# Performance work log

Measured on AMD Instinct MI355X. Metric: run time of the kernel, lower is better.

Reference implementation:

```python
import jax, jax.numpy as jnp
import numpy as np

N_HEAD = 12

def setup_inputs() -> dict:
    key = jax.random.key(0)
    k1, k2, k3, k4, k5 = jax.random.split(key, 5)
    B, T, C = 2, 2048, 768
    x = jax.random.normal(k1, (B, T, C), dtype=jnp.float32)
    W_attn = jax.random.normal(k2, (C, 3 * C), dtype=jnp.float32) * 0.02
    b_attn = jax.random.normal(k3, (3 * C,), dtype=jnp.float32) * 0.02
    W_proj = jax.random.normal(k4, (C, C), dtype=jnp.float32) * 0.02
    b_proj = jax.random.normal(k5, (C,), dtype=jnp.float32) * 0.02
    return {"x": x, "W_attn": W_attn, "b_attn": b_attn, "W_proj": W_proj, "b_proj": b_proj}

def reference(x, W_attn, b_attn, W_proj, b_proj):
    B, T, C = x.shape
    H = N_HEAD
    hd = C // H
    qkv = x @ W_attn + b_attn  # [B,T,3C]
    q, k, v = jnp.split(qkv, 3, axis=2)
    # [B,H,T,hd]
    q = q.reshape(B, T, H, hd).transpose(0, 2, 1, 3)
    k = k.reshape(B, T, H, hd).transpose(0, 2, 1, 3)
    v = v.reshape(B, T, H, hd).transpose(0, 2, 1, 3)
    att = jnp.einsum('bhqd,bhkd->bhqk', q, k) / jnp.sqrt(jnp.float32(hd))
    causal = jnp.tril(jnp.ones((T, T), dtype=bool))
    att = jnp.where(causal[None, None], att, -jnp.inf)
    att = jax.nn.softmax(att, axis=-1)
    y = jnp.einsum('bhqk,bhkd->bhqd', att, v)  # [B,H,T,hd]
    y = y.transpose(0, 2, 1, 3).reshape(B, T, C)
    return y @ W_proj + b_proj
```

## Files before the change

kernel.cpp:

```cpp
#include <hip/hip_runtime.h>
#include <stdint.h>

typedef unsigned short u16;
typedef __attribute__((ext_vector_type(8))) short bf16x8;
typedef __attribute__((ext_vector_type(4))) float f32x4;

__device__ __forceinline__ u16 f2bf(float f){
  union { float f; uint32_t u; } v; v.f = f;
  uint32_t u = v.u;
  u += 0x7FFFu + ((u >> 16) & 1u);
  return (u16)(u >> 16);
}

__device__ __forceinline__ float fexp2(float x){
#if __has_builtin(__builtin_amdgcn_exp2f)
  return __builtin_amdgcn_exp2f(x);
#else
  return exp2f(x);
#endif
}

__device__ __forceinline__ uint32_t cvtpk_bf16(float lo, float hi){
  uint32_t d;
  asm("v_cvt_pk_bf16_f32 %0, %1, %2" : "=v"(d) : "v"(lo), "v"(hi));
  return d;
}

__device__ __forceinline__ f32x4 mfma_bf16(bf16x8 a, bf16x8 b, f32x4 c){
  return __builtin_amdgcn_mfma_f32_16x16x32_bf16(a, b, c, 0, 0, 0);
}

#define QSCALE 0.1803368801111244f

__global__ __launch_bounds__(256) void cast_x_k(const float* __restrict__ x,
                                                u16* __restrict__ xb, int n4){
  int i = blockIdx.x*256 + threadIdx.x;
  if (i >= n4) return;
  float4 v = reinterpret_cast<const float4*>(x)[i];
  uint2 o;
  o.x = (uint32_t)f2bf(v.x) | ((uint32_t)f2bf(v.y) << 16);
  o.y = (uint32_t)f2bf(v.z) | ((uint32_t)f2bf(v.w) << 16);
  reinterpret_cast<uint2*>(xb)[i] = o;
}

__global__ __launch_bounds__(256) void transpose_cast_k(const float* __restrict__ in,
                                                        u16* __restrict__ out,
                                                        int R, int C){
  __shared__ u16 tile[64][66];
  int c0 = blockIdx.x*64, r0 = blockIdx.y*64;
  int tc = threadIdx.x & 63, t4 = threadIdx.x >> 6;
  #pragma unroll
  for (int i=0;i<16;i++){ int r = t4 + i*4; tile[r][tc] = f2bf(in[(size_t)(r0+r)*C + c0 + tc]); }
  __syncthreads();
  #pragma unroll
  for (int i=0;i<16;i++){ int cc = t4 + i*4; out[(size_t)(c0+cc)*R + r0 + tc] = tile[tc][cc]; }
}

#define LDP 40

template<int MFRAG>
__global__ __launch_bounds__(256) void gemm_bf16_k(
    const u16* __restrict__ A, const u16* __restrict__ Bt,
    int M, int N, int K, const float* __restrict__ bias, int mode,
    u16* __restrict__ qo, u16* __restrict__ ko, u16* __restrict__ vo,
    float* __restrict__ fo)
{
  constexpr int BM = MFRAG*32;
  __shared__ u16 As[BM*LDP];
  __shared__ u16 Bs[128*LDP];
  const int m0 = blockIdx.y*BM, n0 = blockIdx.x*128;
  const int tid = threadIdx.x, lane = tid & 63, wid = tid >> 6;
  const int lr = lane & 15, lg = lane >> 4;
  const int wr = wid >> 1, wc = wid & 1;
  f32x4 acc[MFRAG][4] = {};
  const int nk = K >> 5;
  for (int kk = 0; kk < nk; ++kk){
    #pragma unroll
    for (int s = 0; s < MFRAG/2; ++s){
      int ci = tid + 256*s;
      int row = ci >> 2, ch = ci & 3;
      *(uint4*)&As[row*LDP + ch*8] = *(const uint4*)&A[(size_t)(m0+row)*K + kk*32 + ch*8];
    }
    #pragma unroll
    for (int s = 0; s < 2; ++s){
      int ci = tid + 256*s;
      int row = ci >> 2, ch = ci & 3;
      *(uint4*)&Bs[row*LDP + ch*8] = *(const uint4*)&Bt[(size_t)(n0+row)*K + kk*32 + ch*8];
    }
    __syncthreads();
    bf16x8 af[MFRAG], bfr[4];
    #pragma unroll
    for (int m=0;m<MFRAG;m++) af[m] = *(const bf16x8*)&As[(wr*(MFRAG*16) + m*16 + lr)*LDP + lg*8];
    #pragma unroll
    for (int n=0;n<4;n++) bfr[n] = *(const bf16x8*)&Bs[(wc*64 + n*16 + lr)*LDP + lg*8];
    #pragma unroll
    for (int m=0;m<MFRAG;m++)
      #pragma unroll
      for (int n=0;n<4;n++)
        acc[m][n] = mfma_bf16(af[m], bfr[n], acc[m][n]);
    __syncthreads();
  }
  if (mode == 0){
    #pragma unroll
    for (int m=0;m<MFRAG;m++)
      #pragma unroll
      for (int n=0;n<4;n++){
        int gn = n0 + wc*64 + n*16 + lr;
        float bv = bias[gn];
        #pragma unroll
        for (int r=0;r<4;r++){
          int gm = m0 + wr*(MFRAG*16) + m*16 + lg*4 + r;
          fo[(size_t)gm*N + gn] = acc[m][n][r] + bv;
        }
      }
  } else {
    int which = n0 / 768;
    u16* dst = (which==0) ? qo : ko;
    float sc = (which==0) ? QSCALE : 1.0f;
    #pragma unroll
    for (int m=0;m<MFRAG;m++)
      #pragma unroll
      for (int n=0;n<4;n++){
        int gn = n0 + wc*64 + n*16 + lr;
        float bv = bias[gn];
        int cn = gn - which*768;
        int h = cn >> 6, d = cn & 63;
        int gm0 = m0 + wr*(MFRAG*16) + m*16 + lg*4;
        int b = gm0 >> 11, t0 = gm0 & 2047;
        if (which < 2){
          #pragma unroll
          for (int r=0;r<4;r++)
            dst[(size_t)((b*12 + h)*2048 + t0 + r)*64 + d] = f2bf((acc[m][n][r] + bv)*sc);
        } else {
          uint2 o;
          o.x = cvtpk_bf16(acc[m][n][0]+bv, acc[m][n][1]+bv);
          o.y = cvtpk_bf16(acc[m][n][2]+bv, acc[m][n][3]+bv);
          *(uint2*)&vo[((size_t)((b*12 + h)*64 + d))*2048 + t0] = o;
        }
      }
  }
}

__global__ __launch_bounds__(256) void attn_k(
    const u16* __restrict__ qp, const u16* __restrict__ kp,
    const u16* __restrict__ vtp, u16* __restrict__ yp)
{
  __shared__ f32x4 ylh[16][64];
  __shared__ float llh[4][16];
  const int i = blockIdx.x;
  const int bh = i % 24;
  const int qb = 63 - (i / 24);
  const int q0 = qb * 32;
  const int q0A = q0, q0B = q0 + 16;
  const int b = bh / 12, h = bh - b*12;
  const size_t base = (size_t)bh * 131072;
  const int tid = threadIdx.x, lane = tid & 63, wid = tid >> 6;
  const int lr = lane & 15, lg = lane >> 4;
  const int qgA = q0A + lr, qgB = q0B + lr;
  const u16* kbase = kp + base;
  const u16* vbase = vtp + base;

  bf16x8 qfA[2], qfB[2];
  #pragma unroll
  for (int kb=0;kb<2;kb++){
    qfA[kb] = *(const bf16x8*)&qp[base + (size_t)qgA*64 + kb*32 + lg*8];
    qfB[kb] = *(const bf16x8*)&qp[base + (size_t)qgB*64 + kb*32 + lg*8];
  }

  f32x4 yA[4] = {}, yB[4] = {};
  float lA = 0.f, lB = 0.f;
  const float m2 = 8.f;
  const int nt = (qb >> 1) + 1;

  uint32_t ko[8], vo[8];
  #pragma unroll
  for (int nb=0;nb<4;nb++){
    int ke = ((nb&1)*32 + (lr>>2)*8 + (nb>>1)*4 + (lr&3))*64 + lg*8;
    ko[nb*2+0] = (uint32_t)(wid*4096 + ke) * 2u;
    ko[nb*2+1] = (uint32_t)(wid*4096 + ke + 32) * 2u;
  }
  #pragma unroll
  for (int n=0;n<4;n++){
    int ve = (n*16+lr)*2048 + lg*8 + wid*64;
    vo[n*2+0] = (uint32_t)ve * 2u;
    vo[n*2+1] = (uint32_t)(ve + 32) * 2u;
  }

  for (int t = wid; t < nt; t += 4){
    bf16x8 kf[8], vf[8];
    #pragma unroll
    for (int j=0;j<8;j++) kf[j] = *(const bf16x8*)((const char*)kbase + ko[j]);
    #pragma unroll
    for (int j=0;j<8;j++) vf[j] = *(const bf16x8*)((const char*)vbase + vo[j]);
    #pragma unroll
    for (int j=0;j<8;j++){ ko[j] += 32768u; vo[j] += 512u; }

    const int k0 = t*64;
    const int nbmin[4] = {0, 32, 4, 36};

    uint32_t pkA[8], pkB[8];
    auto half_qk = [&](int q0H, int qgH, const bf16x8 (&qfH)[2],
                       float &lH, uint32_t (&pkH)[8]){
      f32x4 s[4] = {};
      __builtin_amdgcn_s_setprio(1);
      if (k0      <= q0H + 15){ s[0]=mfma_bf16(kf[0],qfH[0],s[0]); s[0]=mfma_bf16(kf[1],qfH[1],s[0]); }
      if (k0 + 32 <= q0H + 15){ s[1]=mfma_bf16(kf[2],qfH[0],s[1]); s[1]=mfma_bf16(kf[3],qfH[1],s[1]); }
      if (k0 +  4 <= q0H + 15){ s[2]=mfma_bf16(kf[4],qfH[0],s[2]); s[2]=mfma_bf16(kf[5],qfH[1],s[2]); }
      if (k0 + 36 <= q0H + 15){ s[3]=mfma_bf16(kf[6],qfH[0],s[3]); s[3]=mfma_bf16(kf[7],qfH[1],s[3]); }
      __builtin_amdgcn_s_setprio(0);
      if (k0 + 63 > q0H){
        #pragma unroll
        for (int nb=0;nb<4;nb++){
          int kb0 = k0 + (nb&1)*32 + ((nb>>1)&1)*4 + lg*8;
          #pragma unroll
          for (int r=0;r<4;r++)
            if (kb0 + r > qgH) s[nb][r] = -1e30f;
        }
      }
      float lsum = 0.f;
      #pragma unroll
      for (int nb=0;nb<4;nb++){
        if (k0 + nbmin[nb] <= q0H + 15){
          #pragma unroll
          for (int r=0;r<4;r++){
            float p = fexp2(s[nb][r] - m2);
            s[nb][r] = p;
            lsum += p;
          }
        } else {
          #pragma unroll
          for (int r=0;r<4;r++) s[nb][r] = 0.f;
        }
      }
      lH += lsum;
      #pragma unroll
      for (int nb=0;nb<4;nb++){
        pkH[nb*2]   = cvtpk_bf16(s[nb][0], s[nb][1]);
        pkH[nb*2+1] = cvtpk_bf16(s[nb][2], s[nb][3]);
      }
    };
    half_qk(q0A, qgA, qfA, lA, pkA);
    half_qk(q0B, qgB, qfB, lB, pkB);

    __builtin_amdgcn_s_setprio(1);
    {
      union { uint32_t u[4]; bf16x8 v; } pb;
      pb.u[0]=pkA[0]; pb.u[1]=pkA[1]; pb.u[2]=pkA[4]; pb.u[3]=pkA[5];
      yA[0]=mfma_bf16(vf[0],pb.v,yA[0]); yA[1]=mfma_bf16(vf[2],pb.v,yA[1]);
      yA[2]=mfma_bf16(vf[4],pb.v,yA[2]); yA[3]=mfma_bf16(vf[6],pb.v,yA[3]);
      pb.u[0]=pkA[2]; pb.u[1]=pkA[3]; pb.u[2]=pkA[6]; pb.u[3]=pkA[7];
      yA[0]=mfma_bf16(vf[1],pb.v,yA[0]); yA[1]=mfma_bf16(vf[3],pb.v,yA[1]);
      yA[2]=mfma_bf16(vf[5],pb.v,yA[2]); yA[3]=mfma_bf16(vf[7],pb.v,yA[3]);
      pb.u[0]=pkB[0]; pb.u[1]=pkB[1]; pb.u[2]=pkB[4]; pb.u[3]=pkB[5];
      yB[0]=mfma_bf16(vf[0],pb.v,yB[0]); yB[1]=mfma_bf16(vf[2],pb.v,yB[1]);
      yB[2]=mfma_bf16(vf[4],pb.v,yB[2]); yB[3]=mfma_bf16(vf[6],pb.v,yB[3]);
      pb.u[0]=pkB[2]; pb.u[1]=pkB[3]; pb.u[2]=pkB[6]; pb.u[3]=pkB[7];
      yB[0]=mfma_bf16(vf[1],pb.v,yB[0]); yB[1]=mfma_bf16(vf[3],pb.v,yB[1]);
      yB[2]=mfma_bf16(vf[5],pb.v,yB[2]); yB[3]=mfma_bf16(vf[7],pb.v,yB[3]);
    }
    __builtin_amdgcn_s_setprio(0);
  }

  lA += __shfl_xor(lA, 16);  lA += __shfl_xor(lA, 32);
  lB += __shfl_xor(lB, 16);  lB += __shfl_xor(lB, 32);

  #pragma unroll
  for (int hf=0; hf<2; hf++){
    if (hf) __syncthreads();
    #pragma unroll
    for (int n=0;n<4;n++) ylh[wid*4+n][lane] = hf ? yB[n] : yA[n];
    if (lg == 0) llh[wid][lr] = hf ? lB : lA;
    __syncthreads();
    float Ls = (llh[0][lr] + llh[1][lr]) + (llh[2][lr] + llh[3][lr]);
    f32x4 y0 = ylh[0*4+wid][lane], y1 = ylh[1*4+wid][lane],
          y2 = ylh[2*4+wid][lane], y3 = ylh[3*4+wid][lane];
    f32x4 ys;
    #pragma unroll
    for (int r=0;r<4;r++) ys[r] = (y0[r] + y1[r]) + (y2[r] + y3[r]);
    float inv = 1.0f / Ls;
    uint2 o;
    o.x = cvtpk_bf16(ys[0]*inv, ys[1]*inv);
    o.y = cvtpk_bf16(ys[2]*inv, ys[3]*inv);
    *(uint2*)&yp[(size_t)(b*2048 + q0 + hf*16 + lr)*768 + h*64 + wid*16 + lg*4] = o;
  }
}

extern "C" void kernel_launch(void* const* d_in, const int* in_sizes, int n_in,
                              void* d_out, int out_size, void* d_ws, size_t ws_size,
                              hipStream_t stream)
{
  const float* x  = (const float*)d_in[0];
  const float* Wa = (const float*)d_in[1];
  const float* ba = (const float*)d_in[2];
  const float* Wp = (const float*)d_in[3];
  const float* bp = (const float*)d_in[4];
  float* out = (float*)d_out;
  char* ws = (char*)d_ws;
  u16* xb  = (u16*)(ws + 0);
  u16* wt  = (u16*)(ws + 6291456);
  u16* wpt = (u16*)(ws + 9830400);
  u16* qb  = (u16*)(ws + 11010048);
  u16* kb  = (u16*)(ws + 17301504);
  u16* vtb = (u16*)(ws + 23592960);
  u16* yb  = (u16*)(ws + 29884416);

  cast_x_k<<<3072, 256, 0, stream>>>(x, xb, 786432);
  transpose_cast_k<<<dim3(36,12), 256, 0, stream>>>(Wa, wt, 768, 2304);
  transpose_cast_k<<<dim3(12,12), 256, 0, stream>>>(Wp, wpt, 768, 768);
  gemm_bf16_k<2><<<dim3(18,64), 256, 0, stream>>>(xb, wt, 4096, 2304, 768, ba, 1,
                                                  qb, kb, vtb, nullptr);
  attn_k<<<1536, 256, 0, stream>>>(qb, kb, vtb, yb);
  gemm_bf16_k<2><<<dim3(6,64), 256, 0, stream>>>(yb, wpt, 4096, 768, 768, bp, 0,
                                                 nullptr, nullptr, nullptr, out);
}
```

Baseline: 129.0 us.

## Persistent attention with atomic work queue; merge prep casts into one kernel

The three cast and transpose kernels are merged into a single prep kernel, which also zeroes eight work counters. The attention kernel becomes persistent with 1024 blocks. Each block pulls (query-block, head) tasks from one of eight atomic counters, heaviest query blocks first, so work balances dynamically across CUs instead of relying on a static grid. This adds an atomic and a barrier per task, and makes the attention kernel depend on the counters being reset by the prep kernel.

```diff
diff --git a/kernel.cpp b/kernel.cpp
--- a/kernel.cpp
+++ b/kernel.cpp
@@ -32,23 +32,31 @@
 
 #define QSCALE 0.1803368801111244f
 
-__global__ __launch_bounds__(256) void cast_x_k(const float* __restrict__ x,
-                                                u16* __restrict__ xb, int n4){
-  int i = blockIdx.x*256 + threadIdx.x;
-  if (i >= n4) return;
-  float4 v = reinterpret_cast<const float4*>(x)[i];
-  uint2 o;
-  o.x = (uint32_t)f2bf(v.x) | ((uint32_t)f2bf(v.y) << 16);
-  o.y = (uint32_t)f2bf(v.z) | ((uint32_t)f2bf(v.w) << 16);
-  reinterpret_cast<uint2*>(xb)[i] = o;
-}
-
-__global__ __launch_bounds__(256) void transpose_cast_k(const float* __restrict__ in,
-                                                        u16* __restrict__ out,
-                                                        int R, int C){
+__global__ __launch_bounds__(256) void prep_k(
+    const float* __restrict__ x,  u16* __restrict__ xb,
+    const float* __restrict__ Wa, u16* __restrict__ wt,
+    const float* __restrict__ Wp, u16* __restrict__ wpt,
+    uint32_t* __restrict__ cnt)
+{
   __shared__ u16 tile[64][66];
-  int c0 = blockIdx.x*64, r0 = blockIdx.y*64;
-  int tc = threadIdx.x & 63, t4 = threadIdx.x >> 6;
+  const int bid = blockIdx.x;
+  if (bid < 3072){
+    if (bid == 0 && threadIdx.x < 8) cnt[threadIdx.x] = 0u;
+    int i = bid*256 + threadIdx.x;
+    float4 v = reinterpret_cast<const float4*>(x)[i];
+    uint2 o;
+    o.x = (uint32_t)f2bf(v.x) | ((uint32_t)f2bf(v.y) << 16);
+    o.y = (uint32_t)f2bf(v.z) | ((uint32_t)f2bf(v.w) << 16);
+    reinterpret_cast<uint2*>(xb)[i] = o;
+    return;
+  }
+  const float* in; u16* out; int C, j;
+  if (bid < 3504){ j = bid - 3072; in = Wa; out = wt;  C = 2304; }
+  else           { j = bid - 3504; in = Wp; out = wpt; C = 768;  }
+  const int R = 768;
+  const int nbx = C >> 6;
+  const int c0 = (j % nbx) * 64, r0 = (j / nbx) * 64;
+  const int tc = threadIdx.x & 63, t4 = threadIdx.x >> 6;
   #pragma unroll
   for (int i=0;i<16;i++){ int r = t4 + i*4; tile[r][tc] = f2bf(in[(size_t)(r0+r)*C + c0 + tc]); }
   __syncthreads();
@@ -143,145 +151,160 @@
 
 __global__ __launch_bounds__(256) void attn_k(
     const u16* __restrict__ qp, const u16* __restrict__ kp,
-    const u16* __restrict__ vtp, u16* __restrict__ yp)
+    const u16* __restrict__ vtp, u16* __restrict__ yp,
+    uint32_t* __restrict__ cnt)
 {
   __shared__ f32x4 ylh[16][64];
   __shared__ float llh[4][16];
-  const int i = blockIdx.x;
-  const int bh = i % 24;
-  const int qb = 63 - (i / 24);
-  const int q0 = qb * 32;
-  const int q0A = q0, q0B = q0 + 16;
-  const int b = bh / 12, h = bh - b*12;
-  const size_t base = (size_t)bh * 131072;
+  __shared__ uint32_t task_s;
+  const int qid = blockIdx.x & 7;
   const int tid = threadIdx.x, lane = tid & 63, wid = tid >> 6;
   const int lr = lane & 15, lg = lane >> 4;
-  const int qgA = q0A + lr, qgB = q0B + lr;
-  const u16* kbase = kp + base;
-  const u16* vbase = vtp + base;
-
-  bf16x8 qfA[2], qfB[2];
+
+  int ke[4], ve[4];
   #pragma unroll
-  for (int kb=0;kb<2;kb++){
-    qfA[kb] = *(const bf16x8*)&qp[base + (size_t)qgA*64 + kb*32 + lg*8];
-    qfB[kb] = *(const bf16x8*)&qp[base + (size_t)qgB*64 + kb*32 + lg*8];
-  }
-
-  f32x4 yA[4] = {}, yB[4] = {};
-  float lA = 0.f, lB = 0.f;
-  const float m2 = 8.f;
-  const int nt = (qb >> 1) + 1;
-
-  uint32_t ko[8], vo[8];
+  for (int nb=0;nb<4;nb++)
+    ke[nb] = ((nb&1)*32 + (lr>>2)*8 + ((nb>>1)&1)*4 + (lr&3))*64 + lg*8;
   #pragma unroll
-  for (int nb=0;nb<4;nb++){
-    int ke = ((nb&1)*32 + (lr>>2)*8 + (nb>>1)*4 + (lr&3))*64 + lg*8;
-    ko[nb*2+0] = (uint32_t)(wid*4096 + ke) * 2u;
-    ko[nb*2+1] = (uint32_t)(wid*4096 + ke + 32) * 2u;
-  }
-  #pragma unroll
-  for (int n=0;n<4;n++){
-    int ve = (n*16+lr)*2048 + lg*8 + wid*64;
-    vo[n*2+0] = (uint32_t)ve * 2u;
-    vo[n*2+1] = (uint32_t)(ve + 32) * 2u;
-  }
-
-  for (int t = wid; t < nt; t += 4){
-    bf16x8 kf[8], vf[8];
-    #pragma unroll
-    for (int j=0;j<8;j++) kf[j] = *(const bf16x8*)((const char*)kbase + ko[j]);
-    #pragma unroll
-    for (int j=0;j<8;j++) vf[j] = *(const bf16x8*)((const char*)vbase + vo[j]);
-    #pragma unroll
-    for (int j=0;j<8;j++){ ko[j] += 32768u; vo[j] += 512u; }
-
-    const int k0 = t*64;
-    const int nbmin[4] = {0, 32, 4, 36};
-
-    uint32_t pkA[8], pkB[8];
-    auto half_qk = [&](int q0H, int qgH, const bf16x8 (&qfH)[2],
-                       float &lH, uint32_t (&pkH)[8]){
-      f32x4 s[4] = {};
-      __builtin_amdgcn_s_setprio(1);
-      if (k0      <= q0H + 15){ s[0]=mfma_bf16(kf[0],qfH[0],s[0]); s[0]=mfma_bf16(kf[1],qfH[1],s[0]); }
-      if (k0 + 32 <= q0H + 15){ s[1]=mfma_bf16(kf[2],qfH[0],s[1]); s[1]=mfma_bf16(kf[3],qfH[1],s[1]); }
-      if (k0 +  4 <= q0H + 15){ s[2]=mfma_bf16(kf[4],qfH[0],s[2]); s[2]=mfma_bf16(kf[5],qfH[1],s[2]); }
-      if (k0 + 36 <= q0H + 15){ s[3]=mfma_bf16(kf[6],qfH[0],s[3]); s[3]=mfma_bf16(kf[7],qfH[1],s[3]); }
-      __builtin_amdgcn_s_setprio(0);
-      if (k0 + 63 > q0H){
+  for (int n=0;n<4;n++)
+    ve[n] = (n*16+lr)*2048 + lg*8;
+
+  for (;;){
+    if (tid == 0) task_s = atomicAdd(&cnt[qid], 1u);
+    __syncthreads();
+    const uint32_t m = task_s;
+    if (m >= 192u) return;
+    const int qb = 63 - (int)(m / 3u);
+    const int bh = qid + 8 * (int)(m % 3u);
+    const int q0 = qb * 32;
+    const int q0A = q0, q0B = q0 + 16;
+    const int b = bh / 12, h = bh - b*12;
+    const size_t base = (size_t)bh * 131072;
+    const int qgA = q0A + lr, qgB = q0B + lr;
+    const u16* kbase = kp + base;
+    const u16* vbase = vtp + base;
+
+    bf16x8 qfA[2], qfB[2];
+    #pragma unroll
+    for (int kb=0;kb<2;kb++){
+      qfA[kb] = *(const bf16x8*)&qp[base + (size_t)qgA*64 + kb*32 + lg*8];
+      qfB[kb] = *(const bf16x8*)&qp[base + (size_t)qgB*64 + kb*32 + lg*8];
+    }
+
+    f32x4 yA[4] = {}, yB[4] = {};
+    float lA = 0.f, lB = 0.f;
+    const float m2 = 8.f;
+    const int nt = (qb >> 1) + 1;
+
+    uint32_t ko[8], vo[8];
+    #pragma unroll
+    for (int nb=0;nb<4;nb++){
+      ko[nb*2+0] = (uint32_t)(wid*4096 + ke[nb]) * 2u;
+      ko[nb*2+1] = (uint32_t)(wid*4096 + ke[nb] + 32) * 2u;
+    }
+    #pragma unroll
+    for (int n=0;n<4;n++){
+      vo[n*2+0] = (uint32_t)(ve[n] + wid*64) * 2u;
+      vo[n*2+1] = (uint32_t)(ve[n] + wid*64 + 32) * 2u;
+    }
+
+    for (int t = wid; t < nt; t += 4){
+      bf16x8 kf[8], vf[8];
+      #pragma unroll
+      for (int j=0;j<8;j++) kf[j] = *(const bf16x8*)((const char*)kbase + ko[j]);
+      #pragma unroll
+      for (int j=0;j<8;j++) vf[j] = *(const bf16x8*)((const char*)vbase + vo[j]);
+      #pragma unroll
+      for (int j=0;j<8;j++){ ko[j] += 32768u; vo[j] += 512u; }
+
+      const int k0 = t*64;
+      const int nbmin[4] = {0, 32, 4, 36};
+
+      uint32_t pkA[8], pkB[8];
+      auto half_qk = [&](int q0H, int qgH, const bf16x8 (&qfH)[2],
+                         float &lH, uint32_t (&pkH)[8]){
+        f32x4 s[4] = {};
+        __builtin_amdgcn_s_setprio(1);
+        if (k0      <= q0H + 15){ s[0]=mfma_bf16(kf[0],qfH[0],s[0]); s[0]=mfma_bf16(kf[1],qfH[1],s[0]); }
+        if (k0 + 32 <= q0H + 15){ s[1]=mfma_bf16(kf[2],qfH[0],s[1]); s[1]=mfma_bf16(kf[3],qfH[1],s[1]); }
+        if (k0 +  4 <= q0H + 15){ s[2]=mfma_bf16(kf[4],qfH[0],s[2]); s[2]=mfma_bf16(kf[5],qfH[1],s[2]); }
+        if (k0 + 36 <= q0H + 15){ s[3]=mfma_bf16(kf[6],qfH[0],s[3]); s[3]=mfma_bf16(kf[7],qfH[1],s[3]); }
+        __builtin_amdgcn_s_setprio(0);
+        if (k0 + 63 > q0H){
+          #pragma unroll
+          for (int nb=0;nb<4;nb++){
+            int kb0 = k0 + (nb&1)*32 + ((nb>>1)&1)*4 + lg*8;
+            #pragma unroll
+            for (int r=0;r<4;r++)
+              if (kb0 + r > qgH) s[nb][r] = -1e30f;
+          }
+        }
+        float lsum = 0.f;
         #pragma unroll
         for (int nb=0;nb<4;nb++){
-          int kb0 = k0 + (nb&1)*32 + ((nb>>1)&1)*4 + lg*8;
-          #pragma unroll
-          for (int r=0;r<4;r++)
-            if (kb0 + r > qgH) s[nb][r] = -1e30f;
-        }
+          if (k0 + nbmin[nb] <= q0H + 15){
+            #pragma unroll
+            for (int r=0;r<4;r++){
+              float p = fexp2(s[nb][r] - m2);
+              s[nb][r] = p;
+              lsum += p;
+            }
+          } else {
+            #pragma unroll
+            for (int r=0;r<4;r++) s[nb][r] = 0.f;
+          }
+        }
+        lH += lsum;
+        #pragma unroll
+        for (int nb=0;nb<4;nb++){
+          pkH[nb*2]   = cvtpk_bf16(s[nb][0], s[nb][1]);
+          pkH[nb*2+1] = cvtpk_bf16(s[nb][2], s[nb][3]);
+        }
+      };
+      half_qk(q0A, qgA, qfA, lA, pkA);
+      half_qk(q0B, qgB, qfB, lB, pkB);
+
+      __builtin_amdgcn_s_setprio(1);
+      {
+        union { uint32_t u[4]; bf16x8 v; } pb;
+        pb.u[0]=pkA[0]; pb.u[1]=pkA[1]; pb.u[2]=pkA[4]; pb.u[3]=pkA[5];
+        yA[0]=mfma_bf16(vf[0],pb.v,yA[0]); yA[1]=mfma_bf16(vf[2],pb.v,yA[1]);
+        yA[2]=mfma_bf16(vf[4],pb.v,yA[2]); yA[3]=mfma_bf16(vf[6],pb.v,yA[3]);
+        pb.u[0]=pkA[2]; pb.u[1]=pkA[3]; pb.u[2]=pkA[6]; pb.u[3]=pkA[7];
+        yA[0]=mfma_bf16(vf[1],pb.v,yA[0]); yA[1]=mfma_bf16(vf[3],pb.v,yA[1]);
+        yA[2]=mfma_bf16(vf[5],pb.v,yA[2]); yA[3]=mfma_bf16(vf[7],pb.v,yA[3]);
+        pb.u[0]=pkB[0]; pb.u[1]=pkB[1]; pb.u[2]=pkB[4]; pb.u[3]=pkB[5];
+        yB[0]=mfma_bf16(vf[0],pb.v,yB[0]); yB[1]=mfma_bf16(vf[2],pb.v,yB[1]);
+        yB[2]=mfma_bf16(vf[4],pb.v,yB[2]); yB[3]=mfma_bf16(vf[6],pb.v,yB[3]);
+        pb.u[0]=pkB[2]; pb.u[1]=pkB[3]; pb.u[2]=pkB[6]; pb.u[3]=pkB[7];
+        yB[0]=mfma_bf16(vf[1],pb.v,yB[0]); yB[1]=mfma_bf16(vf[3],pb.v,yB[1]);
+        yB[2]=mfma_bf16(vf[5],pb.v,yB[2]); yB[3]=mfma_bf16(vf[7],pb.v,yB[3]);
       }
-      float lsum = 0.f;
-      #pragma unroll
-      for (int nb=0;nb<4;nb++){
-        if (k0 + nbmin[nb] <= q0H + 15){
-          #pragma unroll
-          for (int r=0;r<4;r++){
-            float p = fexp2(s[nb][r] - m2);
-            s[nb][r] = p;
-            lsum += p;
-          }
-        } else {
-          #pragma unroll
-          for (int r=0;r<4;r++) s[nb][r] = 0.f;
-        }
-      }
-      lH += lsum;
-      #pragma unroll
-      for (int nb=0;nb<4;nb++){
-        pkH[nb*2]   = cvtpk_bf16(s[nb][0], s[nb][1]);
-        pkH[nb*2+1] = cvtpk_bf16(s[nb][2], s[nb][3]);
-      }
-    };
-    half_qk(q0A, qgA, qfA, lA, pkA);
-    half_qk(q0B, qgB, qfB, lB, pkB);
-
-    __builtin_amdgcn_s_setprio(1);
-    {
-      union { uint32_t u[4]; bf16x8 v; } pb;
-      pb.u[0]=pkA[0]; pb.u[1]=pkA[1]; pb.u[2]=pkA[4]; pb.u[3]=pkA[5];
-      yA[0]=mfma_bf16(vf[0],pb.v,yA[0]); yA[1]=mfma_bf16(vf[2],pb.v,yA[1]);
-      yA[2]=mfma_bf16(vf[4],pb.v,yA[2]); yA[3]=mfma_bf16(vf[6],pb.v,yA[3]);
-      pb.u[0]=pkA[2]; pb.u[1]=pkA[3]; pb.u[2]=pkA[6]; pb.u[3]=pkA[7];
-      yA[0]=mfma_bf16(vf[1],pb.v,yA[0]); yA[1]=mfma_bf16(vf[3],pb.v,yA[1]);
-      yA[2]=mfma_bf16(vf[5],pb.v,yA[2]); yA[3]=mfma_bf16(vf[7],pb.v,yA[3]);
-      pb.u[0]=pkB[0]; pb.u[1]=pkB[1]; pb.u[2]=pkB[4]; pb.u[3]=pkB[5];
-      yB[0]=mfma_bf16(vf[0],pb.v,yB[0]); yB[1]=mfma_bf16(vf[2],pb.v,yB[1]);
-      yB[2]=mfma_bf16(vf[4],pb.v,yB[2]); yB[3]=mfma_bf16(vf[6],pb.v,yB[3]);
-      pb.u[0]=pkB[2]; pb.u[1]=pkB[3]; pb.u[2]=pkB[6]; pb.u[3]=pkB[7];
-      yB[0]=mfma_bf16(vf[1],pb.v,yB[0]); yB[1]=mfma_bf16(vf[3],pb.v,yB[1]);
-      yB[2]=mfma_bf16(vf[5],pb.v,yB[2]); yB[3]=mfma_bf16(vf[7],pb.v,yB[3]);
-    }
-    __builtin_amdgcn_s_setprio(0);
-  }
-
-  lA += __shfl_xor(lA, 16);  lA += __shfl_xor(lA, 32);
-  lB += __shfl_xor(lB, 16);  lB += __shfl_xor(lB, 32);
-
-  #pragma unroll
-  for (int hf=0; hf<2; hf++){
-    if (hf) __syncthreads();
-    #pragma unroll
-    for (int n=0;n<4;n++) ylh[wid*4+n][lane] = hf ? yB[n] : yA[n];
-    if (lg == 0) llh[wid][lr] = hf ? lB : lA;
-    __syncthreads();
-    float Ls = (llh[0][lr] + llh[1][lr]) + (llh[2][lr] + llh[3][lr]);
-    f32x4 y0 = ylh[0*4+wid][lane], y1 = ylh[1*4+wid][lane],
-          y2 = ylh[2*4+wid][lane], y3 = ylh[3*4+wid][lane];
-    f32x4 ys;
-    #pragma unroll
-    for (int r=0;r<4;r++) ys[r] = (y0[r] + y1[r]) + (y2[r] + y3[r]);
-    float inv = 1.0f / Ls;
-    uint2 o;
-    o.x = cvtpk_bf16(ys[0]*inv, ys[1]*inv);
-    o.y = cvtpk_bf16(ys[2]*inv, ys[3]*inv);
-    *(uint2*)&yp[(size_t)(b*2048 + q0 + hf*16 + lr)*768 + h*64 + wid*16 + lg*4] = o;
+      __builtin_amdgcn_s_setprio(0);
+    }
+
+    lA += __shfl_xor(lA, 16);  lA += __shfl_xor(lA, 32);
+    lB += __shfl_xor(lB, 16);  lB += __shfl_xor(lB, 32);
+
+    #pragma unroll
+    for (int hf=0; hf<2; hf++){
+      if (hf) __syncthreads();
+      #pragma unroll
+      for (int n=0;n<4;n++) ylh[wid*4+n][lane] = hf ? yB[n] : yA[n];
+      if (lg == 0) llh[wid][lr] = hf ? lB : lA;
+      __syncthreads();
+      float Ls = (llh[0][lr] + llh[1][lr]) + (llh[2][lr] + llh[3][lr]);
+      f32x4 y0 = ylh[0*4+wid][lane], y1 = ylh[1*4+wid][lane],
+            y2 = ylh[2*4+wid][lane], y3 = ylh[3*4+wid][lane];
+      f32x4 ys;
+      #pragma unroll
+      for (int r=0;r<4;r++) ys[r] = (y0[r] + y1[r]) + (y2[r] + y3[r]);
+      float inv = 1.0f / Ls;
+      uint2 o;
+      o.x = cvtpk_bf16(ys[0]*inv, ys[1]*inv);
+      o.y = cvtpk_bf16(ys[2]*inv, ys[3]*inv);
+      *(uint2*)&yp[(size_t)(b*2048 + q0 + hf*16 + lr)*768 + h*64 + wid*16 + lg*4] = o;
+    }
   }
 }
 
@@ -303,13 +326,12 @@
   u16* kb  = (u16*)(ws + 17301504);
   u16* vtb = (u16*)(ws + 23592960);
   u16* yb  = (u16*)(ws + 29884416);
-
-  cast_x_k<<<3072, 256, 0, stream>>>(x, xb, 786432);
-  transpose_cast_k<<<dim3(36,12), 256, 0, stream>>>(Wa, wt, 768, 2304);
-  transpose_cast_k<<<dim3(12,12), 256, 0, stream>>>(Wp, wpt, 768, 768);
+  uint32_t* cnt = (uint32_t*)(ws + 36175872);
+
+  prep_k<<<3648, 256, 0, stream>>>(x, xb, Wa, wt, Wp, wpt, cnt);
   gemm_bf16_k<2><<<dim3(18,64), 256, 0, stream>>>(xb, wt, 4096, 2304, 768, ba, 1,
                                                   qb, kb, vtb, nullptr);
-  attn_k<<<1536, 256, 0, stream>>>(qb, kb, vtb, yb);
+  attn_k<<<1024, 256, 0, stream>>>(qb, kb, vtb, yb, cnt);
   gemm_bf16_k<2><<<dim3(6,64), 256, 0, stream>>>(yb, wpt, 4096, 768, 768, bp, 0,
                                                  nullptr, nullptr, nullptr, out);
 }
```

Result: slower. 136.0 us (+5.5%).
